# Optimization experiments

Measured on AMD Instinct MI355X. Metric: run time of the kernel, lower is better.

Reference implementation:

```python
import jax, jax.numpy as jnp
import numpy as np
from jax import lax

H, I, N, R, K, B, L = 2048, 4096, 16, 128, 4, 1, 2048

def silu(v):
    return v * jax.nn.sigmoid(v)

def setup_inputs() -> dict:
    key = jax.random.key(0)
    ks = jax.random.split(key, 8)
    f = jnp.float32
    x = jax.random.normal(ks[0], (B, L, H), f)
    W_in = jax.random.normal(ks[1], (H, 2 * I), f) / np.sqrt(H).astype(np.float32)
    conv_w = jax.random.normal(ks[2], (I, 1, K), f) / np.sqrt(K).astype(np.float32)  # OIH depthwise
    conv_b = jnp.zeros((I,), f)
    W_x = jax.random.normal(ks[3], (I, R + 2 * N), f) / np.sqrt(I).astype(np.float32)
    W_dt = jax.random.normal(ks[4], (R, I), f) / np.sqrt(R).astype(np.float32)
    # dt bias init as in Mamba: inverse-softplus of log-uniform dt
    dt = jnp.clip(jnp.exp(jax.random.normal(ks[5], (I,), f) * (np.log(0.1) - np.log(0.001)).astype(np.float32) + np.float32(np.log(0.001))), 1e-4, 0.1)
    b_dt = dt + jnp.log(-jnp.expm1(-dt))
    W_out = jax.random.normal(ks[6], (I, H), f) / np.sqrt(I).astype(np.float32)
    A_log = jnp.log(jnp.broadcast_to(jnp.arange(1, N + 1, dtype=f), (I, N)))
    D = jnp.ones((I,), f)
    return {"x": x, "W_in": W_in, "conv_w": conv_w, "conv_b": conv_b, "W_x": W_x,
            "W_dt": W_dt, "b_dt": b_dt, "W_out": W_out, "A_log": A_log, "D": D}

def reference(x, W_in, conv_w, conv_b, W_x, W_dt, b_dt, W_out, A_log, D):
    Bsz, Lq, _ = x.shape
    proj = jnp.swapaxes(x @ W_in, 1, 2)            # [B, 2I, L]
    h, gate = jnp.split(proj, 2, axis=1)           # each [B, I, L]
    # depthwise causal conv1d (pad K-1 both sides, truncate to L)
    h = lax.conv_general_dilated(h, conv_w, (1,), ((K - 1, K - 1),), feature_group_count=I)[..., :Lq]
    h = silu(h + conv_b[None, :, None])            # [B, I, L]
    ssm = jnp.swapaxes(h, 1, 2) @ W_x              # [B, L, R+2N]
    dt, Bm, Cm = jnp.split(ssm, [R, R + N], axis=-1)
    dt = jax.nn.softplus(dt @ W_dt + b_dt)         # [B, L, I]
    dt = jnp.swapaxes(dt, 1, 2)                    # [B, I, L]
    A = -jnp.exp(A_log)                            # [I, N]
    dA = jnp.exp(A[None, :, None, :] * dt[..., None])          # [B, I, L, N]
    dBu = dt[..., None] * Bm[:, None, :, :] * h[..., None]     # [B, I, L, N]

    def step(s, inp):
        dA_t, dBu_t, C_t = inp                     # [B,I,N],[B,I,N],[B,N]
        s = dA_t * s + dBu_t
        y = jnp.einsum('bin,bn->bi', s, C_t)
        return s, y

    s0 = jnp.zeros((Bsz, I, N), x.dtype)
    _, ys = lax.scan(step, s0, (jnp.moveaxis(dA, 2, 0), jnp.moveaxis(dBu, 2, 0), jnp.swapaxes(Cm, 0, 1)))
    y = jnp.moveaxis(ys, 0, 2)                     # [B, I, L]
    y = (y + h * D[None, :, None]) * silu(gate)
    return jnp.swapaxes(y, 1, 2) @ W_out           # [B, L, H]
```

## Files before the change

kernel.cpp:

```cpp
#include <hip/hip_runtime.h>

typedef unsigned short u16;
typedef unsigned int u32;
typedef __attribute__((ext_vector_type(2))) float f32x2;
typedef __attribute__((ext_vector_type(4))) float f32x4;
typedef __attribute__((ext_vector_type(8))) short s16x8;
typedef __attribute__((ext_vector_type(4))) u16 u16x4;

static constexpr int Hdim = 2048, Idim = 4096, Ndim = 16, Rdim = 128, Lseq = 2048;
static constexpr int NCH = 64, LCH = 32;

__device__ __forceinline__ u16 f2bf(float f) {
  u32 u = __builtin_bit_cast(u32, f);
  u += 0x7fffu + ((u >> 16) & 1u);
  return (u16)(u >> 16);
}
__device__ __forceinline__ float bf2f(u16 u) {
  u32 x = ((u32)u) << 16;
  return __builtin_bit_cast(float, x);
}

__global__ void k_cvt(const float* __restrict__ src, u16* __restrict__ dst, int n4) {
  int i = blockIdx.x * blockDim.x + threadIdx.x;
  if (i >= n4) return;
  f32x4 v = ((const f32x4*)src)[i];
  u16x4 o = {f2bf(v.x), f2bf(v.y), f2bf(v.z), f2bf(v.w)};
  ((u16x4*)dst)[i] = o;
}

__global__ void k_tcvt(const float* __restrict__ src, u16* __restrict__ dst,
                       int R, int C, int dstld) {
  __shared__ float tile[32][33];
  int tx = threadIdx.x & 31, ty = threadIdx.x >> 5;
  int c0 = blockIdx.x * 32, r0 = blockIdx.y * 32;
#pragma unroll
  for (int j = 0; j < 32; j += 8) {
    int r = r0 + ty + j, c = c0 + tx;
    tile[ty + j][tx] = (r < R && c < C) ? src[(size_t)r * C + c] : 0.f;
  }
  __syncthreads();
#pragma unroll
  for (int j = 0; j < 32; j += 8) {
    int c = c0 + ty + j, r = r0 + tx;
    if (c < C && r < R) dst[(size_t)c * dstld + r] = f2bf(tile[tx][ty + j]);
  }
}

__global__ __launch_bounds__(256)
void k_tcvt64(const float* __restrict__ src, u16* __restrict__ dst, int C, int ld) {
  __shared__ u16 tile[64][68];
  const int c0 = blockIdx.x * 64, r0 = blockIdx.y * 64;
#pragma unroll
  for (int it = 0; it < 4; ++it) {
    int v = it * 256 + threadIdx.x;
    int row = v >> 4, c4 = v & 15;
    f32x4 d = *(const f32x4*)&src[(size_t)(r0 + row) * C + c0 + c4 * 4];
    u16x4 o = {f2bf(d.x), f2bf(d.y), f2bf(d.z), f2bf(d.w)};
    *(u16x4*)&tile[row][c4 * 4] = o;
  }
  __syncthreads();
#pragma unroll
  for (int it = 0; it < 4; ++it) {
    int v = it * 256 + threadIdx.x;
    int oc = v >> 4, r4 = v & 15;
    u16x4 o = {tile[r4 * 4 + 0][oc], tile[r4 * 4 + 1][oc],
               tile[r4 * 4 + 2][oc], tile[r4 * 4 + 3][oc]};
    *(u16x4*)&dst[(size_t)(c0 + oc) * ld + r0 + r4 * 4] = o;
  }
}

__global__ void k_conv(const u16* __restrict__ projb, const float* __restrict__ cw,
                       const float* __restrict__ cb, u16* __restrict__ hcb) {
  int idx = blockIdx.x * 256 + threadIdx.x;
  int i = idx & (Idim - 1), l = idx >> 12;
  float acc = cb[i];
#pragma unroll
  for (int k = 0; k < 4; ++k) {
    int lk = l - 3 + k;
    if (lk >= 0) acc += cw[i * 4 + k] * bf2f(projb[(size_t)lk * (2 * Idim) + i]);
  }
  float s = acc * (1.f / (1.f + __expf(-acc)));
  hcb[idx] = f2bf(s);
}

__global__ void k_dtr(const float* __restrict__ ssm, u16* __restrict__ dtr) {
  int i = blockIdx.x * blockDim.x + threadIdx.x;
  int l = i >> 5, c4 = i & 31;
  f32x4 v = *(const f32x4*)&ssm[(size_t)l * 256 + c4 * 4];
  u16x4 o = {f2bf(v.x), f2bf(v.y), f2bf(v.z), f2bf(v.w)};
  *(u16x4*)&dtr[(size_t)l * 128 + c4 * 4] = o;
}

__global__ __launch_bounds__(256)
void k_scan1(const u16* __restrict__ dtfb, const u16* __restrict__ hcb,
             const float* __restrict__ ssm, const float* __restrict__ A_log,
             float* __restrict__ Sloc, float* __restrict__ dtsum) {
  __shared__ float Bs[LCH][16];
  const int c = blockIdx.y;
  const int i = blockIdx.x * 256 + threadIdx.x;
  const int l0 = c * LCH;
  {
    int t = threadIdx.x;
    int l = t >> 3, q = t & 7;
    *(f32x2*)&Bs[l][q * 2] = *(const f32x2*)&ssm[(size_t)(l0 + l) * 256 + 128 + q * 2];
  }
  float a[16];
#pragma unroll
  for (int n4 = 0; n4 < 4; ++n4) {
    f32x4 v = *(const f32x4*)&A_log[(size_t)i * 16 + n4 * 4];
    a[n4 * 4 + 0] = -__expf(v.x);
    a[n4 * 4 + 1] = -__expf(v.y);
    a[n4 * 4 + 2] = -__expf(v.z);
    a[n4 * 4 + 3] = -__expf(v.w);
  }
  __syncthreads();
  float s[16];
#pragma unroll
  for (int n = 0; n < 16; ++n) s[n] = 0.f;
  float dsum = 0.f;
  for (int l = 0; l < LCH; ++l) {
    float dtv = bf2f(dtfb[(size_t)(l0 + l) * Idim + i]);
    float hv = bf2f(hcb[(size_t)(l0 + l) * Idim + i]);
    dsum += dtv;
    float dh = dtv * hv;
#pragma unroll
    for (int n = 0; n < 16; ++n) {
      float dA = __expf(a[n] * dtv);
      s[n] = dA * s[n] + dh * Bs[l][n];
    }
  }
#pragma unroll
  for (int n4 = 0; n4 < 4; ++n4) {
    f32x4 v = {s[n4 * 4], s[n4 * 4 + 1], s[n4 * 4 + 2], s[n4 * 4 + 3]};
    *(f32x4*)&Sloc[((size_t)c * Idim + i) * 16 + n4 * 4] = v;
  }
  dtsum[(size_t)c * Idim + i] = dsum;
}

__global__ __launch_bounds__(256)
void k_scan2(const float* __restrict__ Sloc, const float* __restrict__ dtsum,
             const float* __restrict__ A_log, float* __restrict__ sinit) {
  const int idx = blockIdx.x * 256 + threadIdx.x;
  const float a = -__expf(A_log[idx]);
  const int i = idx >> 4;
  float acc = 0.f;
  for (int c = 0; c < NCH; ++c) {
    size_t o = (size_t)c * (Idim * 16) + idx;
    sinit[o] = acc;
    acc = __expf(a * dtsum[(size_t)c * Idim + i]) * acc + Sloc[o];
  }
}

__global__ __launch_bounds__(256)
void k_scan3(const u16* __restrict__ dtfb, const u16* __restrict__ hcb,
             const float* __restrict__ ssm, const float* __restrict__ A_log,
             const float* __restrict__ Dp, const u16* __restrict__ projb,
             const float* __restrict__ sinit, u16* __restrict__ yb) {
  __shared__ float SBC[LCH][32];
  const int c = blockIdx.y;
  const int i = blockIdx.x * 256 + threadIdx.x;
  const int l0 = c * LCH;
  {
    int t = threadIdx.x;
    int l = t >> 3, q = t & 7;
    *(f32x4*)&SBC[l][q * 4] = *(const f32x4*)&ssm[(size_t)(l0 + l) * 256 + 128 + q * 4];
  }
  float a[16], s[16];
#pragma unroll
  for (int n4 = 0; n4 < 4; ++n4) {
    f32x4 v = *(const f32x4*)&A_log[(size_t)i * 16 + n4 * 4];
    a[n4 * 4 + 0] = -__expf(v.x);
    a[n4 * 4 + 1] = -__expf(v.y);
    a[n4 * 4 + 2] = -__expf(v.z);
    a[n4 * 4 + 3] = -__expf(v.w);
    f32x4 sv = *(const f32x4*)&sinit[((size_t)c * Idim + i) * 16 + n4 * 4];
    s[n4 * 4 + 0] = sv.x;
    s[n4 * 4 + 1] = sv.y;
    s[n4 * 4 + 2] = sv.z;
    s[n4 * 4 + 3] = sv.w;
  }
  const float Di = Dp[i];
  __syncthreads();
  for (int l = 0; l < LCH; ++l) {
    float dtv = bf2f(dtfb[(size_t)(l0 + l) * Idim + i]);
    float hv = bf2f(hcb[(size_t)(l0 + l) * Idim + i]);
    float dh = dtv * hv;
    float y = 0.f;
#pragma unroll
    for (int n = 0; n < 16; ++n) {
      float dA = __expf(a[n] * dtv);
      s[n] = dA * s[n] + dh * SBC[l][n];
      y += s[n] * SBC[l][16 + n];
    }
    float g = bf2f(projb[(size_t)(l0 + l) * (2 * Idim) + Idim + i]);
    y = (y + hv * Di) * (g / (1.f + __expf(-g)));
    yb[(size_t)(l0 + l) * Idim + i] = f2bf(y);
  }
}

__device__ __forceinline__ void gload_lds16(const void* g, void* l) {
  __builtin_amdgcn_global_load_lds((const __attribute__((address_space(1))) void*)g,
                                   (__attribute__((address_space(3))) void*)l, 16, 0, 0);
}

template <int EPI>
__device__ __forceinline__ void gemm_body(const u16* __restrict__ A, const u16* __restrict__ Bt,
                                          float* __restrict__ C, u16* __restrict__ Caux,
                                          int N, int K, int kchunk,
                                          const float* __restrict__ bias,
                                          int m0, int n0, int kz) {
  __shared__ u16 As[128 * 32];
  __shared__ u16 Bs[128 * 32];
  const int tid = threadIdx.x;
  const int wave = tid >> 6, lane = tid & 63;
  const int wm = (wave >> 1) * 64, wn = (wave & 1) * 64;
  const int lr = lane >> 2;
  const int lc = lane & 3;
  const int arow = wave * 32;

  f32x4 acc[4][4];
#pragma unroll
  for (int a = 0; a < 4; ++a)
#pragma unroll
    for (int b = 0; b < 4; ++b) acc[a][b] = (f32x4){0.f, 0.f, 0.f, 0.f};

  const int k_begin = kz * kchunk;
  const int k_end = k_begin + kchunk;

  for (int k = k_begin; k < k_end; k += 32) {
#pragma unroll
    for (int j = 0; j < 2; ++j) {
      const u16* ga = A + (size_t)(m0 + arow + j * 16 + lr) * K + k + lc * 8;
      gload_lds16(ga, &As[(arow + j * 16) * 32]);
      const u16* gb = Bt + (size_t)(n0 + arow + j * 16 + lr) * K + k + lc * 8;
      gload_lds16(gb, &Bs[(arow + j * 16) * 32]);
    }
    __syncthreads();
    const int kh = (lane >> 4) * 8;
    const int fr = lane & 15;
    s16x8 af[4], bfr[4];
#pragma unroll
    for (int f = 0; f < 4; ++f) {
      af[f] = *(const s16x8*)&As[(wm + f * 16 + fr) * 32 + kh];
      bfr[f] = *(const s16x8*)&Bs[(wn + f * 16 + fr) * 32 + kh];
    }
#pragma unroll
    for (int fm = 0; fm < 4; ++fm)
#pragma unroll
      for (int fn = 0; fn < 4; ++fn)
        acc[fm][fn] = __builtin_amdgcn_mfma_f32_16x16x32_bf16(af[fm], bfr[fn], acc[fm][fn], 0, 0, 0);
    __syncthreads();
  }

  const int cr = (lane >> 4) * 4, cc = lane & 15;
#pragma unroll
  for (int fm = 0; fm < 4; ++fm)
#pragma unroll
    for (int fn = 0; fn < 4; ++fn)
#pragma unroll
      for (int j = 0; j < 4; ++j) {
        int row = m0 + wm + fm * 16 + cr + j;
        int col = n0 + wn + fn * 16 + cc;
        float v = acc[fm][fn][j];
        if (EPI == 1) {
          atomicAdd(&C[(size_t)row * N + col], v);
        } else {
          float xv = v + bias[col];
          Caux[(size_t)row * N + col] = f2bf(fmaxf(xv, 0.f) + log1pf(__expf(-fabsf(xv))));
        }
      }
}

__global__ __launch_bounds__(256)
void k_gemm3(const u16* __restrict__ A, const u16* __restrict__ Bt, float* __restrict__ C) {
  gemm_body<1>(A, Bt, C, nullptr, 256, Idim, Idim / 8, nullptr,
               blockIdx.x * 128, blockIdx.y * 128, blockIdx.z);
}

__global__ __launch_bounds__(256)
void k_gemm4(const u16* __restrict__ A, const u16* __restrict__ Bt, u16* __restrict__ Caux,
             const float* __restrict__ bias) {
  gemm_body<5>(A, Bt, nullptr, Caux, Idim, Rdim, Rdim, bias,
               blockIdx.x * 128, blockIdx.y * 128, 0);
}

__global__ __launch_bounds__(256)
void k_gemm5(const u16* __restrict__ A, const u16* __restrict__ Bt, float* __restrict__ C) {
  int bid = blockIdx.x;
  int wg = (bid & 7) * 32 + (bid >> 3);
  int m0 = (wg & 15) * 128, n0 = (wg >> 4) * 128;
  gemm_body<1>(A, Bt, C, nullptr, Hdim, Idim, Idim / 2, nullptr, m0, n0, blockIdx.y);
}

static constexpr int G1K = 2048;
static constexpr int G1NT = G1K / 64;
static constexpr int G1NITER = G1NT / 2;

__device__ __forceinline__ void g1_stage(const u16* __restrict__ g, int ld, int row0, int kcol,
                                         u16* lds, int slot, int wid, int lane) {
#pragma unroll
  for (int j = 0; j < 2; ++j) {
    const u16* ga = g + (size_t)(row0 + j * 64 + wid * 8 + (lane >> 3)) * ld
                      + kcol + (((lane & 7) ^ (lane >> 3)) << 3);
    gload_lds16(ga, &lds[slot + j * 4096 + wid * 512]);
  }
}

#define ASLOT(buf, h) (((buf)*2 + (h)) * 8192)
#define BSLOT(buf, h) (32768 + ((buf)*2 + (h)) * 8192)

template <int BUF, int MH, int NH>
__device__ __forceinline__ void g1_compute(const u16* lds, f32x4 (&acc)[2][4][2][2],
                                           int qm, int qn, int lane) {
  const int r16 = lane & 15, kq = lane >> 4;
  s16x8 af[4][2], bq[2][2];
#pragma unroll
  for (int fm = 0; fm < 4; ++fm) {
    int row = qm * 64 + fm * 16 + r16;
#pragma unroll
    for (int ks = 0; ks < 2; ++ks) {
      int ch = (ks * 4 + kq) ^ (row & 7);
      af[fm][ks] = *(const s16x8*)&lds[ASLOT(BUF, MH) + row * 64 + ch * 8];
    }
  }
#pragma unroll
  for (int fn = 0; fn < 2; ++fn) {
    int row = qn * 32 + fn * 16 + r16;
#pragma unroll
    for (int ks = 0; ks < 2; ++ks) {
      int ch = (ks * 4 + kq) ^ (row & 7);
      bq[fn][ks] = *(const s16x8*)&lds[BSLOT(BUF, NH) + row * 64 + ch * 8];
    }
  }
  __builtin_amdgcn_s_setprio(1);
#pragma unroll
  for (int fm = 0; fm < 4; ++fm)
#pragma unroll
    for (int fn = 0; fn < 2; ++fn)
#pragma unroll
      for (int ks = 0; ks < 2; ++ks)
        acc[MH][fm][NH][fn] =
            __builtin_amdgcn_mfma_f32_16x16x32_bf16(af[fm][ks], bq[fn][ks], acc[MH][fm][NH][fn], 0, 0, 0);
  __builtin_amdgcn_s_setprio(0);
}

#define G1BAR()                         \
  do {                                  \
    __builtin_amdgcn_s_barrier();       \
    __builtin_amdgcn_sched_barrier(0);  \
  } while (0)
#define G1VM4() asm volatile("s_waitcnt vmcnt(4)" ::: "memory")

__global__ __launch_bounds__(512, 2)
void k_gemm1_8p(const u16* __restrict__ A, const u16* __restrict__ Bt, u16* __restrict__ Cb) {
  extern __shared__ u16 lds[];
  const int tid = threadIdx.x, wid = tid >> 6, lane = tid & 63;
  const int qm = wid >> 2, qn = wid & 3;
  const int m0 = (int)(blockIdx.x >> 5) * 256, n0 = (int)(blockIdx.x & 31) * 256;

  f32x4 acc[2][4][2][2];
#pragma unroll
  for (int a = 0; a < 2; ++a)
#pragma unroll
    for (int b = 0; b < 4; ++b)
#pragma unroll
      for (int c = 0; c < 2; ++c)
#pragma unroll
        for (int d = 0; d < 2; ++d) acc[a][b][c][d] = (f32x4){0.f, 0.f, 0.f, 0.f};

  g1_stage(A, G1K, m0, 0, lds, ASLOT(0, 0), wid, lane);
  g1_stage(Bt, G1K, n0 + 128, 0, lds, BSLOT(0, 1), wid, lane);
  g1_stage(A, G1K, m0 + 128, 0, lds, ASLOT(0, 1), wid, lane);
  g1_stage(Bt, G1K, n0, 0, lds, BSLOT(0, 0), wid, lane);
  g1_stage(A, G1K, m0, 64, lds, ASLOT(1, 0), wid, lane);
  g1_stage(Bt, G1K, n0 + 128, 64, lds, BSLOT(1, 1), wid, lane);

  for (int i = 0; i < G1NITER - 1; ++i) {
    const int kc0 = i * 128, kc2 = kc0 + 128, kc3 = kc0 + 192;
    g1_stage(A, G1K, m0 + 128, kc0 + 64, lds, ASLOT(1, 1), wid, lane);
    G1VM4();
    G1BAR();
    g1_compute<0, 0, 0>(lds, acc, qm, qn, lane);
    G1BAR();
    g1_stage(Bt, G1K, n0, kc0 + 64, lds, BSLOT(1, 0), wid, lane);
    G1BAR();
    g1_compute<0, 0, 1>(lds, acc, qm, qn, lane);
    G1BAR();
    g1_stage(A, G1K, m0, kc2, lds, ASLOT(0, 0), wid, lane);
    G1BAR();
    g1_compute<0, 1, 1>(lds, acc, qm, qn, lane);
    G1BAR();
    g1_stage(Bt, G1K, n0 + 128, kc2, lds, BSLOT(0, 1), wid, lane);
    G1BAR();
    g1_compute<0, 1, 0>(lds, acc, qm, qn, lane);
    G1BAR();
    g1_stage(A, G1K, m0 + 128, kc2, lds, ASLOT(0, 1), wid, lane);
    G1VM4();
    G1BAR();
    g1_compute<1, 0, 0>(lds, acc, qm, qn, lane);
    G1BAR();
    g1_stage(Bt, G1K, n0, kc2, lds, BSLOT(0, 0), wid, lane);
    G1BAR();
    g1_compute<1, 0, 1>(lds, acc, qm, qn, lane);
    G1BAR();
    g1_stage(A, G1K, m0, kc3, lds, ASLOT(1, 0), wid, lane);
    G1BAR();
    g1_compute<1, 1, 1>(lds, acc, qm, qn, lane);
    G1BAR();
    g1_stage(Bt, G1K, n0 + 128, kc3, lds, BSLOT(1, 1), wid, lane);
    G1BAR();
    g1_compute<1, 1, 0>(lds, acc, qm, qn, lane);
    G1BAR();
  }

  g1_stage(A, G1K, m0 + 128, (G1NT - 1) * 64, lds, ASLOT(1, 1), wid, lane);
  g1_stage(Bt, G1K, n0, (G1NT - 1) * 64, lds, BSLOT(1, 0), wid, lane);
  asm volatile("s_waitcnt vmcnt(0)" ::: "memory");
  G1BAR();
  g1_compute<0, 0, 0>(lds, acc, qm, qn, lane);
  g1_compute<0, 0, 1>(lds, acc, qm, qn, lane);
  g1_compute<0, 1, 1>(lds, acc, qm, qn, lane);
  g1_compute<0, 1, 0>(lds, acc, qm, qn, lane);
  g1_compute<1, 0, 0>(lds, acc, qm, qn, lane);
  g1_compute<1, 0, 1>(lds, acc, qm, qn, lane);
  g1_compute<1, 1, 1>(lds, acc, qm, qn, lane);
  g1_compute<1, 1, 0>(lds, acc, qm, qn, lane);

  const int cr = (lane >> 4) * 4, cc = lane & 15;
#pragma unroll
  for (int mh = 0; mh < 2; ++mh)
#pragma unroll
    for (int fm = 0; fm < 4; ++fm)
#pragma unroll
      for (int nh = 0; nh < 2; ++nh)
#pragma unroll
        for (int fn = 0; fn < 2; ++fn)
#pragma unroll
          for (int j = 0; j < 4; ++j) {
            int row = m0 + mh * 128 + qm * 64 + fm * 16 + cr + j;
            int col = n0 + nh * 128 + qn * 32 + fn * 16 + cc;
            Cb[(size_t)row * 8192 + col] = f2bf(acc[mh][fm][nh][fn][j]);
          }
}

extern "C" void kernel_launch(void* const* d_in, const int* in_sizes, int n_in,
                              void* d_out, int out_size, void* d_ws, size_t ws_size,
                              hipStream_t stream) {
  const float* x = (const float*)d_in[0];
  const float* W_in = (const float*)d_in[1];
  const float* convw = (const float*)d_in[2];
  const float* convb = (const float*)d_in[3];
  const float* W_x = (const float*)d_in[4];
  const float* W_dt = (const float*)d_in[5];
  const float* b_dt = (const float*)d_in[6];
  const float* W_out = (const float*)d_in[7];
  const float* A_log = (const float*)d_in[8];
  const float* Dp = (const float*)d_in[9];
  float* out = (float*)d_out;

  char* w = (char*)d_ws;
  const size_t OFF_PROJ = 0;
  const size_t OFF_HC = OFF_PROJ + (size_t)Lseq * 2 * Idim * 4;
  const size_t OFF_DT = OFF_HC + (size_t)Lseq * Idim * 4;
  const size_t OFF_XB = OFF_DT + (size_t)Lseq * Idim * 4;
  const size_t OFF_WIN = OFF_XB + (size_t)Lseq * Hdim * 2;
  const size_t OFF_WOUT = OFF_WIN + (size_t)2 * Idim * Hdim * 2;
  const size_t OFF_HCB = OFF_WOUT + (size_t)Hdim * Idim * 2;
  const size_t OFF_YB = OFF_HCB + (size_t)Lseq * Idim * 2;
  const size_t OFF_WX = OFF_YB + (size_t)Lseq * Idim * 2;
  const size_t OFF_WDT = OFF_WX + (size_t)256 * Idim * 2;
  const size_t OFF_SSM = OFF_WDT + (size_t)Idim * Rdim * 2;
  const size_t OFF_DTR = OFF_SSM + (size_t)Lseq * 256 * 4;

  u16* projb = (u16*)(w + OFF_PROJ);
  u16* dtfb = (u16*)(w + OFF_DT);
  u16* xb = (u16*)(w + OFF_XB);
  u16* winT = (u16*)(w + OFF_WIN);
  u16* woutT = (u16*)(w + OFF_WOUT);
  u16* hcb = (u16*)(w + OFF_HCB);
  u16* yb = (u16*)(w + OFF_YB);
  u16* wxt = (u16*)(w + OFF_WX);
  u16* wdtT = (u16*)(w + OFF_WDT);
  float* ssm = (float*)(w + OFF_SSM);
  u16* dtr = (u16*)(w + OFF_DTR);
  float* Sloc = (float*)(w + OFF_HC);
  float* sinit = (float*)(w + OFF_WIN);
  float* dtsum = (float*)(w + OFF_WIN + (size_t)16 * 1024 * 1024);

  hipMemsetAsync(wxt, 0, (size_t)(OFF_SSM - OFF_WX) + (size_t)Lseq * 256 * 4, stream);
  hipMemsetAsync(out, 0, (size_t)Lseq * Hdim * 4, stream);

  k_cvt<<<(Lseq * Hdim / 4 + 255) / 256, 256, 0, stream>>>(x, xb, Lseq * Hdim / 4);
  k_tcvt64<<<dim3(2 * Idim / 64, Hdim / 64), 256, 0, stream>>>(W_in, winT, 2 * Idim, Hdim);
  k_tcvt<<<dim3(5, Idim / 32), 256, 0, stream>>>(W_x, wxt, Idim, 160, Idim);
  k_tcvt64<<<dim3(Idim / 64, Rdim / 64), 256, 0, stream>>>(W_dt, wdtT, Idim, Rdim);
  k_tcvt64<<<dim3(Hdim / 64, Idim / 64), 256, 0, stream>>>(W_out, woutT, Hdim, Idim);

  hipFuncSetAttribute((const void*)k_gemm1_8p, hipFuncAttributeMaxDynamicSharedMemorySize, 131072);
  k_gemm1_8p<<<256, 512, 131072, stream>>>(xb, winT, projb);

  k_conv<<<(size_t)Lseq * Idim / 256, 256, 0, stream>>>(projb, convw, convb, hcb);

  k_gemm3<<<dim3(Lseq / 128, 2, 8), 256, 0, stream>>>(hcb, wxt, ssm);

  k_dtr<<<Lseq * 32 / 256, 256, 0, stream>>>(ssm, dtr);

  k_gemm4<<<dim3(Lseq / 128, Idim / 128), 256, 0, stream>>>(dtr, wdtT, dtfb, b_dt);

  k_scan1<<<dim3(Idim / 256, NCH), 256, 0, stream>>>(dtfb, hcb, ssm, A_log, Sloc, dtsum);
  k_scan2<<<Idim * 16 / 256, 256, 0, stream>>>(Sloc, dtsum, A_log, sinit);
  k_scan3<<<dim3(Idim / 256, NCH), 256, 0, stream>>>(dtfb, hcb, ssm, A_log, Dp, projb, sinit, yb);

  k_gemm5<<<dim3(256, 2), 256, 0, stream>>>(yb, woutT, out);
}
```

Before: 480.5 us.

## Replace atomic split-K with partial buffers plus reduction; reuse 256x256 GEMM for output projection

The output projection GEMM now reuses the 512-thread, 256x256-tile pipelined kernel from the input projection. It is templated over K stride and iteration count and runs with 4-way split-K. Both split-K GEMMs (x_proj and out_proj) write fp32 partials to workspace instead of doing atomicAdd, and separate reduction kernels sum them. This removes the memsets of out and ssm, and the reduction for x_proj also produces the bf16 dt input, so the old k_dtr kernel is dropped. In exchange it costs extra launches and roughly 64MB of partial-buffer traffic for the output GEMM.

Result: faster. 459.4 us (-4.4%).

```diff
diff --git a/kernel.cpp b/kernel.cpp
--- a/kernel.cpp
+++ b/kernel.cpp
@@ -83,12 +83,34 @@
   hcb[idx] = f2bf(s);
 }
 
-__global__ void k_dtr(const float* __restrict__ ssm, u16* __restrict__ dtr) {
-  int i = blockIdx.x * blockDim.x + threadIdx.x;
-  int l = i >> 5, c4 = i & 31;
-  f32x4 v = *(const f32x4*)&ssm[(size_t)l * 256 + c4 * 4];
-  u16x4 o = {f2bf(v.x), f2bf(v.y), f2bf(v.z), f2bf(v.w)};
-  *(u16x4*)&dtr[(size_t)l * 128 + c4 * 4] = o;
+__global__ __launch_bounds__(256)
+void k_red3(const float* __restrict__ Cp, float* __restrict__ ssm, u16* __restrict__ dtr) {
+  int i = blockIdx.x * 256 + threadIdx.x;
+  f32x4 s = {0.f, 0.f, 0.f, 0.f};
+#pragma unroll
+  for (int z = 0; z < 8; ++z) {
+    f32x4 v = ((const f32x4*)(Cp + (size_t)z * Lseq * 256))[i];
+    s.x += v.x; s.y += v.y; s.z += v.z; s.w += v.w;
+  }
+  ((f32x4*)ssm)[i] = s;
+  int l = i >> 6, c4 = i & 63;
+  if (c4 < 32) {
+    u16x4 o = {f2bf(s.x), f2bf(s.y), f2bf(s.z), f2bf(s.w)};
+    *(u16x4*)&dtr[(size_t)l * 128 + c4 * 4] = o;
+  }
+}
+
+__global__ __launch_bounds__(256)
+void k_red5(const float* __restrict__ Cp, float* __restrict__ out) {
+  int i = blockIdx.x * 256 + threadIdx.x;
+  const size_t S = (size_t)Lseq * Hdim;
+  f32x4 a = ((const f32x4*)Cp)[i];
+  f32x4 b = ((const f32x4*)(Cp + S))[i];
+  f32x4 c = ((const f32x4*)(Cp + 2 * S))[i];
+  f32x4 d = ((const f32x4*)(Cp + 3 * S))[i];
+  f32x4 r = {(a.x + b.x) + (c.x + d.x), (a.y + b.y) + (c.y + d.y),
+             (a.z + b.z) + (c.z + d.z), (a.w + b.w) + (c.w + d.w)};
+  ((f32x4*)out)[i] = r;
 }
 
 __global__ __launch_bounds__(256)
@@ -262,8 +284,8 @@
         int row = m0 + wm + fm * 16 + cr + j;
         int col = n0 + wn + fn * 16 + cc;
         float v = acc[fm][fn][j];
-        if (EPI == 1) {
-          atomicAdd(&C[(size_t)row * N + col], v);
+        if (EPI == 0) {
+          C[(size_t)row * N + col] = v;
         } else {
           float xv = v + bias[col];
           Caux[(size_t)row * N + col] = f2bf(fmaxf(xv, 0.f) + log1pf(__expf(-fabsf(xv))));
@@ -272,9 +294,9 @@
 }
 
 __global__ __launch_bounds__(256)
-void k_gemm3(const u16* __restrict__ A, const u16* __restrict__ Bt, float* __restrict__ C) {
-  gemm_body<1>(A, Bt, C, nullptr, 256, Idim, Idim / 8, nullptr,
-               blockIdx.x * 128, blockIdx.y * 128, blockIdx.z);
+void k_gemm3(const u16* __restrict__ A, const u16* __restrict__ Bt, float* __restrict__ Cp) {
+  gemm_body<0>(A, Bt, Cp + (size_t)blockIdx.z * Lseq * 256, nullptr, 256, Idim, Idim / 8,
+               nullptr, blockIdx.x * 128, blockIdx.y * 128, blockIdx.z);
 }
 
 __global__ __launch_bounds__(256)
@@ -284,19 +306,7 @@
                blockIdx.x * 128, blockIdx.y * 128, 0);
 }
 
-__global__ __launch_bounds__(256)
-void k_gemm5(const u16* __restrict__ A, const u16* __restrict__ Bt, float* __restrict__ C) {
-  int bid = blockIdx.x;
-  int wg = (bid & 7) * 32 + (bid >> 3);
-  int m0 = (wg & 15) * 128, n0 = (wg >> 4) * 128;
-  gemm_body<1>(A, Bt, C, nullptr, Hdim, Idim, Idim / 2, nullptr, m0, n0, blockIdx.y);
-}
-
-static constexpr int G1K = 2048;
-static constexpr int G1NT = G1K / 64;
-static constexpr int G1NITER = G1NT / 2;
-
-__device__ __forceinline__ void g1_stage(const u16* __restrict__ g, int ld, int row0, int kcol,
+__device__ __forceinline__ void g8_stage(const u16* __restrict__ g, int ld, int row0, int kcol,
                                          u16* lds, int slot, int wid, int lane) {
 #pragma unroll
   for (int j = 0; j < 2; ++j) {
@@ -310,7 +320,7 @@
 #define BSLOT(buf, h) (32768 + ((buf)*2 + (h)) * 8192)
 
 template <int BUF, int MH, int NH>
-__device__ __forceinline__ void g1_compute(const u16* lds, f32x4 (&acc)[2][4][2][2],
+__device__ __forceinline__ void g8_compute(const u16* lds, f32x4 (&acc)[2][4][2][2],
                                            int qm, int qn, int lane) {
   const int r16 = lane & 15, kq = lane >> 4;
   s16x8 af[4][2], bq[2][2];
@@ -344,19 +354,20 @@
   __builtin_amdgcn_s_setprio(0);
 }
 
-#define G1BAR()                         \
+#define G8BAR()                         \
   do {                                  \
     __builtin_amdgcn_s_barrier();       \
     __builtin_amdgcn_sched_barrier(0);  \
   } while (0)
-#define G1VM4() asm volatile("s_waitcnt vmcnt(4)" ::: "memory")
-
-__global__ __launch_bounds__(512, 2)
-void k_gemm1_8p(const u16* __restrict__ A, const u16* __restrict__ Bt, u16* __restrict__ Cb) {
+#define G8VM4() asm volatile("s_waitcnt vmcnt(4)" ::: "memory")
+
+template <int KLD, int NITER, int OUTLD, int EPI>
+__device__ __forceinline__ void g8p_body(const u16* __restrict__ A, const u16* __restrict__ Bt,
+                                         float* __restrict__ Cf, u16* __restrict__ Cb,
+                                         int m0, int n0, int kbase) {
   extern __shared__ u16 lds[];
   const int tid = threadIdx.x, wid = tid >> 6, lane = tid & 63;
   const int qm = wid >> 2, qn = wid & 3;
-  const int m0 = (int)(blockIdx.x >> 5) * 256, n0 = (int)(blockIdx.x & 31) * 256;
 
   f32x4 acc[2][4][2][2];
 #pragma unroll
@@ -368,63 +379,63 @@
 #pragma unroll
         for (int d = 0; d < 2; ++d) acc[a][b][c][d] = (f32x4){0.f, 0.f, 0.f, 0.f};
 
-  g1_stage(A, G1K, m0, 0, lds, ASLOT(0, 0), wid, lane);
-  g1_stage(Bt, G1K, n0 + 128, 0, lds, BSLOT(0, 1), wid, lane);
-  g1_stage(A, G1K, m0 + 128, 0, lds, ASLOT(0, 1), wid, lane);
-  g1_stage(Bt, G1K, n0, 0, lds, BSLOT(0, 0), wid, lane);
-  g1_stage(A, G1K, m0, 64, lds, ASLOT(1, 0), wid, lane);
-  g1_stage(Bt, G1K, n0 + 128, 64, lds, BSLOT(1, 1), wid, lane);
-
-  for (int i = 0; i < G1NITER - 1; ++i) {
-    const int kc0 = i * 128, kc2 = kc0 + 128, kc3 = kc0 + 192;
-    g1_stage(A, G1K, m0 + 128, kc0 + 64, lds, ASLOT(1, 1), wid, lane);
-    G1VM4();
-    G1BAR();
-    g1_compute<0, 0, 0>(lds, acc, qm, qn, lane);
-    G1BAR();
-    g1_stage(Bt, G1K, n0, kc0 + 64, lds, BSLOT(1, 0), wid, lane);
-    G1BAR();
-    g1_compute<0, 0, 1>(lds, acc, qm, qn, lane);
-    G1BAR();
-    g1_stage(A, G1K, m0, kc2, lds, ASLOT(0, 0), wid, lane);
-    G1BAR();
-    g1_compute<0, 1, 1>(lds, acc, qm, qn, lane);
-    G1BAR();
-    g1_stage(Bt, G1K, n0 + 128, kc2, lds, BSLOT(0, 1), wid, lane);
-    G1BAR();
-    g1_compute<0, 1, 0>(lds, acc, qm, qn, lane);
-    G1BAR();
-    g1_stage(A, G1K, m0 + 128, kc2, lds, ASLOT(0, 1), wid, lane);
-    G1VM4();
-    G1BAR();
-    g1_compute<1, 0, 0>(lds, acc, qm, qn, lane);
-    G1BAR();
-    g1_stage(Bt, G1K, n0, kc2, lds, BSLOT(0, 0), wid, lane);
-    G1BAR();
-    g1_compute<1, 0, 1>(lds, acc, qm, qn, lane);
-    G1BAR();
-    g1_stage(A, G1K, m0, kc3, lds, ASLOT(1, 0), wid, lane);
-    G1BAR();
-    g1_compute<1, 1, 1>(lds, acc, qm, qn, lane);
-    G1BAR();
-    g1_stage(Bt, G1K, n0 + 128, kc3, lds, BSLOT(1, 1), wid, lane);
-    G1BAR();
-    g1_compute<1, 1, 0>(lds, acc, qm, qn, lane);
-    G1BAR();
-  }
-
-  g1_stage(A, G1K, m0 + 128, (G1NT - 1) * 64, lds, ASLOT(1, 1), wid, lane);
-  g1_stage(Bt, G1K, n0, (G1NT - 1) * 64, lds, BSLOT(1, 0), wid, lane);
+  g8_stage(A, KLD, m0, kbase, lds, ASLOT(0, 0), wid, lane);
+  g8_stage(Bt, KLD, n0 + 128, kbase, lds, BSLOT(0, 1), wid, lane);
+  g8_stage(A, KLD, m0 + 128, kbase, lds, ASLOT(0, 1), wid, lane);
+  g8_stage(Bt, KLD, n0, kbase, lds, BSLOT(0, 0), wid, lane);
+  g8_stage(A, KLD, m0, kbase + 64, lds, ASLOT(1, 0), wid, lane);
+  g8_stage(Bt, KLD, n0 + 128, kbase + 64, lds, BSLOT(1, 1), wid, lane);
+
+  for (int i = 0; i < NITER - 1; ++i) {
+    const int kc0 = kbase + i * 128, kc2 = kc0 + 128, kc3 = kc0 + 192;
+    g8_stage(A, KLD, m0 + 128, kc0 + 64, lds, ASLOT(1, 1), wid, lane);
+    G8VM4();
+    G8BAR();
+    g8_compute<0, 0, 0>(lds, acc, qm, qn, lane);
+    G8BAR();
+    g8_stage(Bt, KLD, n0, kc0 + 64, lds, BSLOT(1, 0), wid, lane);
+    G8BAR();
+    g8_compute<0, 0, 1>(lds, acc, qm, qn, lane);
+    G8BAR();
+    g8_stage(A, KLD, m0, kc2, lds, ASLOT(0, 0), wid, lane);
+    G8BAR();
+    g8_compute<0, 1, 1>(lds, acc, qm, qn, lane);
+    G8BAR();
+    g8_stage(Bt, KLD, n0 + 128, kc2, lds, BSLOT(0, 1), wid, lane);
+    G8BAR();
+    g8_compute<0, 1, 0>(lds, acc, qm, qn, lane);
+    G8BAR();
+    g8_stage(A, KLD, m0 + 128, kc2, lds, ASLOT(0, 1), wid, lane);
+    G8VM4();
+    G8BAR();
+    g8_compute<1, 0, 0>(lds, acc, qm, qn, lane);
+    G8BAR();
+    g8_stage(Bt, KLD, n0, kc2, lds, BSLOT(0, 0), wid, lane);
+    G8BAR();
+    g8_compute<1, 0, 1>(lds, acc, qm, qn, lane);
+    G8BAR();
+    g8_stage(A, KLD, m0, kc3, lds, ASLOT(1, 0), wid, lane);
+    G8BAR();
+    g8_compute<1, 1, 1>(lds, acc, qm, qn, lane);
+    G8BAR();
+    g8_stage(Bt, KLD, n0 + 128, kc3, lds, BSLOT(1, 1), wid, lane);
+    G8BAR();
+    g8_compute<1, 1, 0>(lds, acc, qm, qn, lane);
+    G8BAR();
+  }
+
+  g8_stage(A, KLD, m0 + 128, kbase + (2 * NITER - 1) * 64, lds, ASLOT(1, 1), wid, lane);
+  g8_stage(Bt, KLD, n0, kbase + (2 * NITER - 1) * 64, lds, BSLOT(1, 0), wid, lane);
   asm volatile("s_waitcnt vmcnt(0)" ::: "memory");
-  G1BAR();
-  g1_compute<0, 0, 0>(lds, acc, qm, qn, lane);
-  g1_compute<0, 0, 1>(lds, acc, qm, qn, lane);
-  g1_compute<0, 1, 1>(lds, acc, qm, qn, lane);
-  g1_compute<0, 1, 0>(lds, acc, qm, qn, lane);
-  g1_compute<1, 0, 0>(lds, acc, qm, qn, lane);
-  g1_compute<1, 0, 1>(lds, acc, qm, qn, lane);
-  g1_compute<1, 1, 1>(lds, acc, qm, qn, lane);
-  g1_compute<1, 1, 0>(lds, acc, qm, qn, lane);
+  G8BAR();
+  g8_compute<0, 0, 0>(lds, acc, qm, qn, lane);
+  g8_compute<0, 0, 1>(lds, acc, qm, qn, lane);
+  g8_compute<0, 1, 1>(lds, acc, qm, qn, lane);
+  g8_compute<0, 1, 0>(lds, acc, qm, qn, lane);
+  g8_compute<1, 0, 0>(lds, acc, qm, qn, lane);
+  g8_compute<1, 0, 1>(lds, acc, qm, qn, lane);
+  g8_compute<1, 1, 1>(lds, acc, qm, qn, lane);
+  g8_compute<1, 1, 0>(lds, acc, qm, qn, lane);
 
   const int cr = (lane >> 4) * 4, cc = lane & 15;
 #pragma unroll
@@ -439,8 +450,25 @@
           for (int j = 0; j < 4; ++j) {
             int row = m0 + mh * 128 + qm * 64 + fm * 16 + cr + j;
             int col = n0 + nh * 128 + qn * 32 + fn * 16 + cc;
-            Cb[(size_t)row * 8192 + col] = f2bf(acc[mh][fm][nh][fn][j]);
+            float v = acc[mh][fm][nh][fn][j];
+            if (EPI == 0) Cb[(size_t)row * OUTLD + col] = f2bf(v);
+            else Cf[(size_t)row * OUTLD + col] = v;
           }
+}
+
+__global__ __launch_bounds__(512, 2)
+void k_gemm1_8p(const u16* __restrict__ A, const u16* __restrict__ Bt, u16* __restrict__ Cb) {
+  const int m0 = (int)(blockIdx.x >> 5) * 256, n0 = (int)(blockIdx.x & 31) * 256;
+  g8p_body<2048, 16, 8192, 0>(A, Bt, nullptr, Cb, m0, n0, 0);
+}
+
+__global__ __launch_bounds__(512, 2)
+void k_gemm5_8p(const u16* __restrict__ A, const u16* __restrict__ Bt, float* __restrict__ Cp) {
+  int bid = blockIdx.x;
+  int wg = (bid & 7) * 8 + (bid >> 3);
+  int m0 = (wg >> 3) * 256, n0 = (wg & 7) * 256;
+  float* Cf = Cp + (size_t)blockIdx.y * Lseq * Hdim;
+  g8p_body<4096, 8, 2048, 1>(A, Bt, Cf, nullptr, m0, n0, (int)blockIdx.y * 1024);
 }
 
 extern "C" void kernel_launch(void* const* d_in, const int* in_sizes, int n_in,
@@ -483,12 +511,13 @@
   u16* wdtT = (u16*)(w + OFF_WDT);
   float* ssm = (float*)(w + OFF_SSM);
   u16* dtr = (u16*)(w + OFF_DTR);
+  float* Cpart3 = (float*)(w + OFF_HC);
   float* Sloc = (float*)(w + OFF_HC);
   float* sinit = (float*)(w + OFF_WIN);
   float* dtsum = (float*)(w + OFF_WIN + (size_t)16 * 1024 * 1024);
-
-  hipMemsetAsync(wxt, 0, (size_t)(OFF_SSM - OFF_WX) + (size_t)Lseq * 256 * 4, stream);
-  hipMemsetAsync(out, 0, (size_t)Lseq * Hdim * 4, stream);
+  float* Cpart5 = (float*)(w + OFF_PROJ);
+
+  hipMemsetAsync(wxt, 0, (size_t)256 * Idim * 2, stream);
 
   k_cvt<<<(Lseq * Hdim / 4 + 255) / 256, 256, 0, stream>>>(x, xb, Lseq * Hdim / 4);
   k_tcvt64<<<dim3(2 * Idim / 64, Hdim / 64), 256, 0, stream>>>(W_in, winT, 2 * Idim, Hdim);
@@ -501,9 +530,8 @@
 
   k_conv<<<(size_t)Lseq * Idim / 256, 256, 0, stream>>>(projb, convw, convb, hcb);
 
-  k_gemm3<<<dim3(Lseq / 128, 2, 8), 256, 0, stream>>>(hcb, wxt, ssm);
-
-  k_dtr<<<Lseq * 32 / 256, 256, 0, stream>>>(ssm, dtr);
+  k_gemm3<<<dim3(Lseq / 128, 2, 8), 256, 0, stream>>>(hcb, wxt, Cpart3);
+  k_red3<<<Lseq * 64 / 256, 256, 0, stream>>>(Cpart3, ssm, dtr);
 
   k_gemm4<<<dim3(Lseq / 128, Idim / 128), 256, 0, stream>>>(dtr, wdtT, dtfb, b_dt);
 
@@ -511,5 +539,7 @@
   k_scan2<<<Idim * 16 / 256, 256, 0, stream>>>(Sloc, dtsum, A_log, sinit);
   k_scan3<<<dim3(Idim / 256, NCH), 256, 0, stream>>>(dtfb, hcb, ssm, A_log, Dp, projb, sinit, yb);
 
-  k_gemm5<<<dim3(256, 2), 256, 0, stream>>>(yb, woutT, out);
-}
+  hipFuncSetAttribute((const void*)k_gemm5_8p, hipFuncAttributeMaxDynamicSharedMemorySize, 131072);
+  k_gemm5_8p<<<dim3(64, 4), 512, 131072, stream>>>(yb, woutT, Cpart5);
+  k_red5<<<Lseq * Hdim / 4 / 256, 256, 0, stream>>>(Cpart5, out);
+}
```
